# Kernel tuning notes

Measured on AMD Instinct MI355X. Metric: run time of the kernel, lower is better.

The kernel has to match this reference:

```python
import jax, jax.numpy as jnp
import numpy as np

# ---- config (from init_kwargs) ----
BASE_SIZE = 16
RATIOS = np.array([0.5, 1.0, 2.0])
N_LAYERS = 3
SCALES = 2.0 ** np.arange(N_LAYERS)
STRIDE = 16
PRE_NMS_TOPN = 2000
POST_NMS_TOPN = 300
MIN_THRESHOLD = 16.0
NMS_THRESH = 0.7
IMG_W = 1024
IMG_H = 1024
B, H, W = 16, 64, 64
A = len(RATIOS) * len(SCALES)  # 9


def _whctrs(a):
    w = a[2] - a[0] + 1.0
    h = a[3] - a[1] + 1.0
    return w, h, a[0] + 0.5 * (w - 1.0), a[1] + 0.5 * (h - 1.0)


def _mkanchors(ws, hs, cx, cy):
    return np.stack([cx - 0.5 * (ws - 1.0), cy - 0.5 * (hs - 1.0),
                     cx + 0.5 * (ws - 1.0), cy + 0.5 * (hs - 1.0)], axis=1)


def _generate_anchors():
    base = np.array([0.0, 0.0, BASE_SIZE - 1.0, BASE_SIZE - 1.0])
    w, h, cx, cy = _whctrs(base)
    size = w * h
    ws = np.round(np.sqrt(size / RATIOS))
    hs = np.round(ws * RATIOS)
    ratio_anchors = _mkanchors(ws, hs, np.full_like(ws, cx), np.full_like(ws, cy))
    out = []
    for ra in ratio_anchors:
        rw, rh, rcx, rcy = _whctrs(ra)
        out.append(_mkanchors(rw * SCALES, rh * SCALES,
                              np.full_like(SCALES, rcx), np.full_like(SCALES, rcy)))
    return np.concatenate(out, axis=0)  # (A, 4)


def _all_anchors(height, width):
    anchors = _generate_anchors()  # (A, 4)
    sx = np.arange(width) * STRIDE
    sy = np.arange(height) * STRIDE
    sx, sy = np.meshgrid(sx, sy)  # (H, W) row-major over y -> matches permute(0,2,3,1)
    shifts = np.stack([sx.ravel(), sy.ravel(), sx.ravel(), sy.ravel()], axis=1)  # (K, 4)
    return (anchors[None, :, :] + shifts[:, None, :]).reshape(-1, 4).astype(np.float32)  # (K*A, 4)


def _decode(deltas, anchors):
    # bbox_reg_to_coord: standard bbox_transform_inv
    aw = anchors[:, 2] - anchors[:, 0] + 1.0
    ah = anchors[:, 3] - anchors[:, 1] + 1.0
    acx = anchors[:, 0] + 0.5 * aw
    acy = anchors[:, 1] + 0.5 * ah
    cx = deltas[..., 0] * aw + acx
    cy = deltas[..., 1] * ah + acy
    pw = jnp.exp(deltas[..., 2]) * aw
    ph = jnp.exp(deltas[..., 3]) * ah
    return jnp.stack([cx - 0.5 * pw, cy - 0.5 * ph,
                      cx + 0.5 * pw, cy + 0.5 * ph], axis=-1)


def _nms_single(boxes, scores):
    # boxes: (N, 4) sorted by descending score
    N = boxes.shape[0]
    x1, y1, x2, y2 = boxes[:, 0], boxes[:, 1], boxes[:, 2], boxes[:, 3]
    areas = (x2 - x1 + 1.0) * (y2 - y1 + 1.0)
    iw = jnp.maximum(0.0, jnp.minimum(x2[:, None], x2[None, :]) - jnp.maximum(x1[:, None], x1[None, :]) + 1.0)
    ih = jnp.maximum(0.0, jnp.minimum(y2[:, None], y2[None, :]) - jnp.maximum(y1[:, None], y1[None, :]) + 1.0)
    inter = iw * ih
    iou = inter / (areas[:, None] + areas[None, :] - inter)  # (N, N)
    idx = jnp.arange(N)

    def body(sup, i):  # greedy sequential NMS
        keep_i = ~sup[i]
        sup = sup | (keep_i & (iou[i] > NMS_THRESH) & (idx > i))
        return sup, keep_i

    _, keep = jax.lax.scan(body, jnp.zeros(N, dtype=bool), idx)
    # kept boxes first, preserving score order; fixed-size output padded with zeros
    prio = jnp.where(keep, idx, idx + N)
    order = jnp.argsort(prio)[:POST_NMS_TOPN]
    valid = keep[order]
    out_boxes = jnp.where(valid[:, None], boxes[order], 0.0)
    out_scores = jnp.where(valid, scores[order], 0.0)
    return out_boxes, out_scores


def reference(labels_pred, bbox_reg):
    b, _, h, w = labels_pred.shape
    anchors = jnp.asarray(_all_anchors(h, w))  # (K*A, 4)
    scores = labels_pred.transpose(0, 2, 3, 1).reshape(b, -1, 2)[..., 1]  # (B, K*A)
    deltas = bbox_reg.transpose(0, 2, 3, 1).reshape(b, -1, 4)  # (B, K*A, 4)
    boxes = _decode(deltas, anchors)
    boxes = jnp.stack([
        jnp.clip(boxes[..., 0], 0.0, IMG_W - 1.0),
        jnp.clip(boxes[..., 1], 0.0, IMG_H - 1.0),
        jnp.clip(boxes[..., 2], 0.0, IMG_W - 1.0),
        jnp.clip(boxes[..., 3], 0.0, IMG_H - 1.0)], axis=-1)
    keep = ((boxes[..., 2] - boxes[..., 0] + 1.0 >= MIN_THRESHOLD)
            & (boxes[..., 3] - boxes[..., 1] + 1.0 >= MIN_THRESHOLD))
    masked = jnp.where(keep, scores, -jnp.inf)
    top_scores, top_idx = jax.lax.top_k(masked, PRE_NMS_TOPN)  # (B, pre)
    top_boxes = jnp.take_along_axis(boxes, top_idx[..., None], axis=1)  # (B, pre, 4)
    return jax.vmap(_nms_single)(top_boxes, top_scores)


def setup_inputs() -> dict:
    key = jax.random.key(0)
    k1, k2 = jax.random.split(key)
    labels_pred = jax.random.normal(k1, (B, 2 * A, H, W), dtype=jnp.float32)
    bbox_reg = jax.random.normal(k2, (B, 4 * A, H, W), dtype=jnp.float32) * 0.2
    return {"labels_pred": labels_pred, "bbox_reg": bbox_reg}
```

## Files before the change

kernel.cpp:

```cpp
#include <hip/hip_runtime.h>
#include <stdint.h>

#pragma clang fp contract(off)

typedef unsigned long long ull;

#define NB 16
#define NA 9
#define HW 4096
#define NANCH (NA*HW)
#define TOTAL (NB*NANCH)
#define TOPN 2000
#define PADN 2048
#define SELPAD 3072
#define OUTN 300
#define HBITS 13
#define HBINS (1 << HBITS)
#define MNMS 384
#define MSTRIPS (MNMS/64)
#define MPITCH 8
#define GD2 16

#define MIDC 0x1.666667p-1

__constant__ float c_ax1[9] = {-3.5f,-15.f,-38.f,  0.f, -8.f,-24.f,  2.5f, -3.f,-14.f};
__constant__ float c_ay1[9] = { 2.f,  -4.f,-16.f,  0.f, -8.f,-24.f, -3.f,-14.f,-36.f};
__constant__ float c_ax2[9] = {18.5f, 30.f, 53.f, 15.f, 23.f, 39.f, 12.5f, 18.f, 29.f};
__constant__ float c_ay2[9] = {13.f,  19.f, 31.f, 15.f, 23.f, 39.f, 18.f,  29.f, 51.f};

__device__ __forceinline__ void decode_box(int a, int x, int y,
    float d0, float d1, float d2, float d3,
    float& x1, float& y1, float& x2, float& y2) {
  float ax1 = c_ax1[a] + 16.f * (float)x;
  float ay1 = c_ay1[a] + 16.f * (float)y;
  float ax2 = c_ax2[a] + 16.f * (float)x;
  float ay2 = c_ay2[a] + 16.f * (float)y;
  float aw  = ax2 - ax1 + 1.f;
  float ah  = ay2 - ay1 + 1.f;
  float acx = ax1 + 0.5f * aw;
  float acy = ay1 + 0.5f * ah;
  float cx = d0 * aw + acx;
  float cy = d1 * ah + acy;
  float pw = expf(d2) * aw;
  float ph = expf(d3) * ah;
  x1 = cx - 0.5f * pw;
  y1 = cy - 0.5f * ph;
  x2 = cx + 0.5f * pw;
  y2 = cy + 0.5f * ph;
  x1 = fminf(fmaxf(x1, 0.f), 1023.f);
  y1 = fminf(fmaxf(y1, 0.f), 1023.f);
  x2 = fminf(fmaxf(x2, 0.f), 1023.f);
  y2 = fminf(fmaxf(y2, 0.f), 1023.f);
}

__device__ __forceinline__ uint32_t f2ord(float f) {
  uint32_t u = __float_as_uint(f);
  return (u & 0x80000000u) ? ~u : (u | 0x80000000u);
}
__device__ __forceinline__ float ord2f(uint32_t u) {
  return (u & 0x80000000u) ? __uint_as_float(u ^ 0x80000000u) : __uint_as_float(~u);
}

__global__ void k_score(const float* __restrict__ labels, const float* __restrict__ bbox,
                        uint32_t* __restrict__ keys) {
  int t = blockIdx.x * 256 + threadIdx.x;
  if (t >= TOTAL) return;
  int pos = t & (HW - 1);
  int ba  = t >> 12;
  int a = ba % 9, b = ba / 9;
  float score = labels[((b * 18 + 2 * a + 1) << 12) + pos];
  const float* dp = bbox + ((b * 36 + 4 * a) << 12) + pos;
  float d0 = dp[0], d1 = dp[4096], d2 = dp[8192], d3 = dp[12288];
  int y = pos >> 6, x = pos & 63;
  float x1, y1, x2, y2;
  decode_box(a, x, y, d0, d1, d2, d3, x1, y1, x2, y2);
  bool keep = (x2 - x1 + 1.f >= 16.f) && (y2 - y1 + 1.f >= 16.f);
  float s = keep ? score : -INFINITY;
  keys[t] = f2ord(s);
}

__global__ __launch_bounds__(1024) void k_batch(const uint32_t* __restrict__ keys,
                                                ull* __restrict__ selKeys,
                                                uint32_t* __restrict__ counters) {
  int b = blockIdx.x, tid = threadIdx.x;
  int wave = tid >> 6, lane = tid & 63;
  __shared__ uint32_t hist[HBINS];
  __shared__ uint32_t wtot[16];
  __shared__ uint32_t sh_T, sh_cnt;
  const uint32_t* kb = keys + b * NANCH;
  const uint4* kb4 = (const uint4*)kb;
#pragma unroll
  for (int k = 0; k < HBINS / 1024; ++k) hist[k * 1024 + tid] = 0u;
  if (tid == 0) { sh_T = 0u; sh_cnt = 0u; }
  __syncthreads();
  for (int i4 = tid; i4 < NANCH / 4; i4 += 1024) {
    uint4 v = kb4[i4];
    if (v.x & 0x80000000u) atomicAdd(&hist[v.x >> (32 - HBITS)], 1u);
    if (v.y & 0x80000000u) atomicAdd(&hist[v.y >> (32 - HBITS)], 1u);
    if (v.z & 0x80000000u) atomicAdd(&hist[v.z >> (32 - HBITS)], 1u);
    if (v.w & 0x80000000u) atomicAdd(&hist[v.w >> (32 - HBITS)], 1u);
  }
  __syncthreads();
  uint32_t c[8], suf[8];
#pragma unroll
  for (int k = 0; k < 8; ++k) c[k] = hist[tid * 8 + k];
  suf[7] = c[7];
#pragma unroll
  for (int k = 6; k >= 0; --k) suf[k] = c[k] + suf[k + 1];
  uint32_t total = suf[0];
  uint32_t wsuf = total;
#pragma unroll
  for (int off = 1; off < 64; off <<= 1) {
    uint32_t v = __shfl_down(wsuf, off);
    if (lane + off < 64) wsuf += v;
  }
  if (lane == 0) wtot[wave] = wsuf;
  __syncthreads();
  uint32_t wab = 0;
  for (int w = wave + 1; w < 16; ++w) wab += wtot[w];
  uint32_t ssum = wsuf + wab;
  uint32_t above_t = ssum - total;
  if (above_t < TOPN && ssum >= TOPN) {
    uint32_t T = (uint32_t)(tid * 8);
#pragma unroll
    for (int k = 7; k >= 0; --k) {
      uint32_t ab = above_t + ((k < 7) ? suf[k + 1] : 0u);
      if (ab < TOPN && ab + c[k] >= TOPN) T = (uint32_t)(tid * 8 + k);
    }
    sh_T = T;
  }
  __syncthreads();
  uint32_t T = sh_T;
  for (int i4 = tid; i4 < NANCH / 4; i4 += 1024) {
    uint4 v = kb4[i4];
    uint32_t vv[4] = { v.x, v.y, v.z, v.w };
#pragma unroll
    for (int cc = 0; cc < 4; ++cc) {
      uint32_t u = vv[cc];
      if ((u >> (32 - HBITS)) >= T) {
        uint32_t slot = atomicAdd(&sh_cnt, 1u);
        if (slot < SELPAD) {
          int i = i4 * 4 + cc;
          uint32_t canon = (uint32_t)((i & 4095) * 9 + (i >> 12));
          selKeys[b * SELPAD + slot] = (((ull)(~u)) << 32) | canon;
        }
      }
    }
  }
  __syncthreads();
  if (tid == 0) counters[b] = (sh_cnt < SELPAD) ? sh_cnt : SELPAD;
}

__global__ __launch_bounds__(256) void k_rank(const ull* __restrict__ selKeys,
                        const uint32_t* __restrict__ counters, const float* __restrict__ bbox,
                        float4* __restrict__ boxes, float* __restrict__ areas,
                        float* __restrict__ selScore) {
  int b = blockIdx.y;
  int i = blockIdx.x * 256 + threadIdx.x;
  int tid = threadIdx.x;
  uint32_t n = counters[b];
  const ull* sk = selKeys + b * SELPAD;
  ull ki = (i < (int)n) ? sk[i] : ~0ull;
  int rank = 0;
  __shared__ ull chunk[256];
  for (uint32_t base = 0; base < n; base += 256) {
    uint32_t j = base + (uint32_t)tid;
    chunk[tid] = (j < n) ? sk[j] : ~0ull;
    __syncthreads();
    int lim = (int)(n - base < 256u ? n - base : 256u);
    for (int t2 = 0; t2 < lim; ++t2) rank += (chunk[t2] < ki) ? 1 : 0;
    __syncthreads();
  }
  if (i < (int)n && rank < TOPN) {
    uint32_t idx = (uint32_t)ki;
    selScore[b * TOPN + rank] = ord2f(~((uint32_t)(ki >> 32)));
    int pos = (int)idx / 9, a = (int)idx - 9 * pos;
    int y = pos >> 6, x = pos & 63;
    const float* dp = bbox + ((b * 36 + 4 * a) << 12) + pos;
    float d0 = dp[0], d1 = dp[4096], d2 = dp[8192], d3 = dp[12288];
    float x1, y1, x2, y2;
    decode_box(a, x, y, d0, d1, d2, d3, x1, y1, x2, y2);
    boxes[b * PADN + rank] = make_float4(x1, y1, x2, y2);
    areas[b * PADN + rank] = (x2 - x1 + 1.f) * (y2 - y1 + 1.f);
  }
}

__global__ __launch_bounds__(256) void k_mask(const float4* __restrict__ boxes,
                                              const float* __restrict__ areas,
                                              ull* __restrict__ gmask) {
  int rb = blockIdx.x, b = blockIdx.y;
  int tid = threadIdx.x, wv = tid >> 6, lane = tid & 63;
  int rbase = rb * 32;
  int smin = rbase >> 6;
  __shared__ float4 sRow[32];
  __shared__ float  sAr[32];
  if (tid < 32) {
    sRow[tid] = boxes[b * PADN + rbase + tid];
    sAr[tid]  = areas[b * PADN + rbase + tid];
  }
  float4 bj[MSTRIPS];
  float  ja[MSTRIPS];
#pragma unroll
  for (int s = 0; s < MSTRIPS; ++s) {
    if (s >= smin) {
      bj[s] = boxes[b * PADN + (s << 6) + lane];
      ja[s] = areas[b * PADN + (s << 6) + lane];
    }
  }
  __syncthreads();
  const double MD = MIDC;
  for (int r = wv; r < 32; r += 4) {
    int i = rbase + r;
    float4 bi = sRow[r];
    float  ia = sAr[r];
#pragma unroll
    for (int s = 0; s < MSTRIPS; ++s) {
      if (s < smin) continue;
      int j = (s << 6) + lane;
      float iw = fminf(bi.z, bj[s].z) - fmaxf(bi.x, bj[s].x) + 1.f; iw = fmaxf(iw, 0.f);
      float ih = fminf(bi.w, bj[s].w) - fmaxf(bi.y, bj[s].y) + 1.f; ih = fmaxf(ih, 0.f);
      float inter = iw * ih;
      float uu = (ia + ja[s]) - inter;
      bool sup = (j > i) && ((double)inter >= MD * (double)uu);
      ull mb = __ballot(sup);
      if (lane == 0) gmask[((size_t)b * MNMS + i) * MPITCH + s] = mb;
    }
  }
}

__global__ __launch_bounds__(64) void k_scan(const ull* __restrict__ gmask,
                                             const float4* __restrict__ boxes,
                                             const float* __restrict__ areas,
                                             const float* __restrict__ selScore,
                                             float* __restrict__ out) {
  int b = blockIdx.x, lane = threadIdx.x;
  const ull* mb = gmask + (size_t)b * MNMS * MPITCH;
  int l8 = lane & 7;
  __shared__ int kidx[OUTN];
  __shared__ int sh_cnt;
  const double MD = MIDC;
  ull supw = 0ull;
  int cnt = 0;
  ull pf[GD2];
#pragma unroll
  for (int ph = 0; ph < GD2; ++ph) pf[ph] = mb[ph * MPITCH + l8];
  for (int base = 0; base < MNMS && cnt < OUTN; base += GD2) {
#pragma unroll
    for (int ph = 0; ph < GD2; ++ph) {
      int i = base + ph;
      ull bal = __ballot(((supw >> (i & 63)) & 1ull) != 0ull);
      if (!((bal >> (i >> 6)) & 1ull)) {
        ull mm = (l8 >= (i >> 6) && l8 < MSTRIPS) ? pf[ph] : 0ull;
        supw |= mm;
        if (lane == 0 && cnt < OUTN) kidx[cnt] = i;
        cnt++;
      }
      int nx = i + GD2; if (nx > MNMS - 1) nx = MNMS - 1;
      pf[ph] = mb[nx * MPITCH + l8];
    }
  }
  for (int i = MNMS; i < TOPN && cnt < OUTN; ++i) {
    float4 bi = boxes[b * PADN + i];
    float ia = areas[b * PADN + i];
    bool sup = false;
    for (int cb = 0; cb < cnt; cb += 64) {
      int k = cb + lane;
      if (k < cnt) {
        int kj = kidx[k];
        float4 bk = boxes[b * PADN + kj];
        float ka = areas[b * PADN + kj];
        float iw = fminf(bi.z, bk.z) - fmaxf(bi.x, bk.x) + 1.f; iw = fmaxf(iw, 0.f);
        float ih = fminf(bi.w, bk.w) - fmaxf(bi.y, bk.y) + 1.f; ih = fmaxf(ih, 0.f);
        float inter = iw * ih;
        float uu = (ia + ka) - inter;
        sup = sup || ((double)inter >= MD * (double)uu);
      }
    }
    if (!__any(sup)) {
      if (lane == 0) kidx[cnt] = i;
      cnt++;
    }
  }
  if (lane == 0) sh_cnt = (cnt < OUTN) ? cnt : OUTN;
  __syncthreads();
  int c = sh_cnt;
  float4* ob = (float4*)out;
  for (int s2 = lane; s2 < OUTN; s2 += 64) {
    float4 bx = make_float4(0.f, 0.f, 0.f, 0.f);
    float sc = 0.f;
    if (s2 < c) {
      int i = kidx[s2];
      bx = boxes[b * PADN + i];
      sc = selScore[b * TOPN + i];
    }
    ob[b * OUTN + s2] = bx;
    out[NB * OUTN * 4 + b * OUTN + s2] = sc;
  }
}

extern "C" void kernel_launch(void* const* d_in, const int* in_sizes, int n_in,
                              void* d_out, int out_size, void* d_ws, size_t ws_size,
                              hipStream_t stream) {
  const float* labels = (const float*)d_in[0];
  const float* bbox   = (const float*)d_in[1];
  char* ws = (char*)d_ws;
  uint32_t* keys    = (uint32_t*)(ws + 0);
  ull* selKeys      = (ull*)(ws + 2359296);
  float* selScore   = (float*)(ws + 2752512);
  float* areas      = (float*)(ws + 2880512);
  float4* boxes     = (float4*)(ws + 3011584);
  uint32_t* counters= (uint32_t*)(ws + 3535872);
  ull* gmask        = (ull*)(ws + 3535936);
  float* out = (float*)d_out;

  hipLaunchKernelGGL(k_score, dim3((TOTAL + 255) / 256), dim3(256), 0, stream, labels, bbox, keys);
  hipLaunchKernelGGL(k_batch, dim3(NB), dim3(1024), 0, stream, keys, selKeys, counters);
  hipLaunchKernelGGL(k_rank,  dim3(SELPAD / 256, NB), dim3(256), 0, stream, selKeys, counters, bbox, boxes, areas, selScore);
  hipLaunchKernelGGL(k_mask,  dim3(MNMS / 32, NB), dim3(256), 0, stream, boxes, areas, gmask);
  hipLaunchKernelGGL(k_scan,  dim3(NB), dim3(64), 0, stream, gmask, boxes, areas, selScore, out);
}
```

Before: 90.42 us.

## Compute full NMS suppression bitmask for all 2000 boxes and scan it

Extends the parallel IoU bitmask kernel from the first 384 candidates to all 2000 (63 row blocks times 32 column strips) and removes the serial fallback loop that tested later candidates against kept boxes one by one. The scan kernel now walks 32-bit mask words held across lanes and uses a shuffle to read the suppression bit, with a software prefetch of upcoming rows. This trades a much larger mask computation and about 8 MB of mask traffic for removing the slow serial tail in the scan. The mask workspace grows substantially and must fit in the workspace buffer.

Measured after the change: 146.6 us. 1.62x slower.

```diff
diff --git a/kernel.cpp b/kernel.cpp
--- a/kernel.cpp
+++ b/kernel.cpp
@@ -16,10 +16,9 @@
 #define OUTN 300
 #define HBITS 13
 #define HBINS (1 << HBITS)
-#define MNMS 384
-#define MSTRIPS (MNMS/64)
-#define MPITCH 8
-#define GD2 16
+#define MROWS 2048
+#define MW 32
+#define GDS 16
 
 #define MIDC 0x1.666667p-1
 
@@ -198,87 +197,54 @@
     sRow[tid] = boxes[b * PADN + rbase + tid];
     sAr[tid]  = areas[b * PADN + rbase + tid];
   }
-  float4 bj[MSTRIPS];
-  float  ja[MSTRIPS];
-#pragma unroll
-  for (int s = 0; s < MSTRIPS; ++s) {
-    if (s >= smin) {
-      bj[s] = boxes[b * PADN + (s << 6) + lane];
-      ja[s] = areas[b * PADN + (s << 6) + lane];
-    }
-  }
   __syncthreads();
   const double MD = MIDC;
-  for (int r = wv; r < 32; r += 4) {
-    int i = rbase + r;
-    float4 bi = sRow[r];
-    float  ia = sAr[r];
-#pragma unroll
-    for (int s = 0; s < MSTRIPS; ++s) {
-      if (s < smin) continue;
-      int j = (s << 6) + lane;
-      float iw = fminf(bi.z, bj[s].z) - fmaxf(bi.x, bj[s].x) + 1.f; iw = fmaxf(iw, 0.f);
-      float ih = fminf(bi.w, bj[s].w) - fmaxf(bi.y, bj[s].y) + 1.f; ih = fmaxf(ih, 0.f);
+  for (int s = smin; s < 32; ++s) {
+    int j = (s << 6) + lane;
+    float4 bj = boxes[b * PADN + j];
+    float  ja = areas[b * PADN + j];
+    bool jvalid = (j < TOPN);
+    for (int r = wv; r < 32; r += 4) {
+      int i = rbase + r;
+      float4 bi = sRow[r];
+      float  ia = sAr[r];
+      float iw = fminf(bi.z, bj.z) - fmaxf(bi.x, bj.x) + 1.f; iw = fmaxf(iw, 0.f);
+      float ih = fminf(bi.w, bj.w) - fmaxf(bi.y, bj.y) + 1.f; ih = fmaxf(ih, 0.f);
       float inter = iw * ih;
-      float uu = (ia + ja[s]) - inter;
-      bool sup = (j > i) && ((double)inter >= MD * (double)uu);
+      float uu = (ia + ja) - inter;
+      bool sup = jvalid && (j > i) && ((double)inter >= MD * (double)uu);
       ull mb = __ballot(sup);
-      if (lane == 0) gmask[((size_t)b * MNMS + i) * MPITCH + s] = mb;
+      if (lane == 0 && i < TOPN) gmask[((size_t)b * MROWS + i) * MW + s] = mb;
     }
   }
 }
 
 __global__ __launch_bounds__(64) void k_scan(const ull* __restrict__ gmask,
                                              const float4* __restrict__ boxes,
-                                             const float* __restrict__ areas,
                                              const float* __restrict__ selScore,
                                              float* __restrict__ out) {
   int b = blockIdx.x, lane = threadIdx.x;
-  const ull* mb = gmask + (size_t)b * MNMS * MPITCH;
-  int l8 = lane & 7;
+  const uint32_t* mrows = (const uint32_t*)(gmask + (size_t)b * MROWS * MW);
   __shared__ int kidx[OUTN];
   __shared__ int sh_cnt;
-  const double MD = MIDC;
-  ull supw = 0ull;
+  uint32_t m[GDS];
+#pragma unroll
+  for (int ph = 0; ph < GDS; ++ph) m[ph] = mrows[ph * 64 + lane];
+  uint32_t supw = 0u;
   int cnt = 0;
-  ull pf[GD2];
-#pragma unroll
-  for (int ph = 0; ph < GD2; ++ph) pf[ph] = mb[ph * MPITCH + l8];
-  for (int base = 0; base < MNMS && cnt < OUTN; base += GD2) {
-#pragma unroll
-    for (int ph = 0; ph < GD2; ++ph) {
+  for (int base = 0; base < TOPN && cnt < OUTN; base += GDS) {
+#pragma unroll
+    for (int ph = 0; ph < GDS; ++ph) {
       int i = base + ph;
-      ull bal = __ballot(((supw >> (i & 63)) & 1ull) != 0ull);
-      if (!((bal >> (i >> 6)) & 1ull)) {
-        ull mm = (l8 >= (i >> 6) && l8 < MSTRIPS) ? pf[ph] : 0ull;
+      uint32_t sw = __shfl(supw, i >> 5);
+      if (!((sw >> (i & 31)) & 1u)) {
+        uint32_t mm = (lane >= (uint32_t)((i >> 6) << 1)) ? m[ph] : 0u;
         supw |= mm;
         if (lane == 0 && cnt < OUTN) kidx[cnt] = i;
         cnt++;
       }
-      int nx = i + GD2; if (nx > MNMS - 1) nx = MNMS - 1;
-      pf[ph] = mb[nx * MPITCH + l8];
-    }
-  }
-  for (int i = MNMS; i < TOPN && cnt < OUTN; ++i) {
-    float4 bi = boxes[b * PADN + i];
-    float ia = areas[b * PADN + i];
-    bool sup = false;
-    for (int cb = 0; cb < cnt; cb += 64) {
-      int k = cb + lane;
-      if (k < cnt) {
-        int kj = kidx[k];
-        float4 bk = boxes[b * PADN + kj];
-        float ka = areas[b * PADN + kj];
-        float iw = fminf(bi.z, bk.z) - fmaxf(bi.x, bk.x) + 1.f; iw = fmaxf(iw, 0.f);
-        float ih = fminf(bi.w, bk.w) - fmaxf(bi.y, bk.y) + 1.f; ih = fmaxf(ih, 0.f);
-        float inter = iw * ih;
-        float uu = (ia + ka) - inter;
-        sup = sup || ((double)inter >= MD * (double)uu);
-      }
-    }
-    if (!__any(sup)) {
-      if (lane == 0) kidx[cnt] = i;
-      cnt++;
+      int nx = i + GDS; if (nx > TOPN - 1) nx = TOPN - 1;
+      m[ph] = mrows[nx * 64 + lane];
     }
   }
   if (lane == 0) sh_cnt = (cnt < OUTN) ? cnt : OUTN;
@@ -316,6 +282,6 @@
   hipLaunchKernelGGL(k_score, dim3((TOTAL + 255) / 256), dim3(256), 0, stream, labels, bbox, keys);
   hipLaunchKernelGGL(k_batch, dim3(NB), dim3(1024), 0, stream, keys, selKeys, counters);
   hipLaunchKernelGGL(k_rank,  dim3(SELPAD / 256, NB), dim3(256), 0, stream, selKeys, counters, bbox, boxes, areas, selScore);
-  hipLaunchKernelGGL(k_mask,  dim3(MNMS / 32, NB), dim3(256), 0, stream, boxes, areas, gmask);
-  hipLaunchKernelGGL(k_scan,  dim3(NB), dim3(64), 0, stream, gmask, boxes, areas, selScore, out);
-}
+  hipLaunchKernelGGL(k_mask,  dim3(63, NB), dim3(256), 0, stream, boxes, areas, gmask);
+  hipLaunchKernelGGL(k_scan,  dim3(NB), dim3(64), 0, stream, gmask, boxes, selScore, out);
+}
```
